# Kernel tuning notes

Hardware: AMD Instinct MI355X
Metric: run time of the kernel (lower is better)

The kernel has to match this reference:

```python
import jax, jax.numpy as jnp
import numpy as np

N_NODES = 50000
N_EDGES = 400000
IN, HID, OUT = 256, 64, 64
HEADS = (8, 8, 1)
NEG_SLOPE = 0.2


def setup_inputs() -> dict:
    key = jax.random.key(0)
    ks = jax.random.split(key, 16)
    def lin(k, fi, fo):
        return jax.random.normal(k, (fi, fo), jnp.float32) / np.sqrt(fi)
    H0, H1, H2 = HEADS
    return {
        "x": jax.random.normal(ks[0], (N_NODES, IN), jnp.float32),
        "src": jax.random.randint(ks[1], (N_EDGES,), 0, N_NODES),
        "dst": jax.random.randint(ks[2], (N_EDGES,), 0, N_NODES),
        # layer 0: in=256 -> (8 heads, 64)
        "W1": lin(ks[3], IN, H0 * HID),
        "al1": 0.1 * jax.random.normal(ks[4], (H0, HID), jnp.float32),
        "ar1": 0.1 * jax.random.normal(ks[5], (H0, HID), jnp.float32),
        "b1": jnp.zeros((H0 * HID,), jnp.float32),
        # layer 1: in=512 -> (8 heads, 64), identity residual (512 == 8*64)
        "W2": lin(ks[6], H0 * HID, H1 * HID),
        "al2": 0.1 * jax.random.normal(ks[7], (H1, HID), jnp.float32),
        "ar2": 0.1 * jax.random.normal(ks[8], (H1, HID), jnp.float32),
        "b2": jnp.zeros((H1 * HID,), jnp.float32),
        # layer 2: in=512 -> (1 head, 64), linear residual projection
        "W3": lin(ks[9], H1 * HID, H2 * OUT),
        "al3": 0.1 * jax.random.normal(ks[10], (H2, OUT), jnp.float32),
        "ar3": 0.1 * jax.random.normal(ks[11], (H2, OUT), jnp.float32),
        "b3": jnp.zeros((H2 * OUT,), jnp.float32),
        "Wr3": lin(ks[12], H1 * HID, H2 * OUT),
    }


def _gat_conv(h, src, dst, W, al, ar, b, res, act):
    # DGL GATConv on a homogeneous graph (feat_src == feat_dst).
    N = h.shape[0]
    H, D = al.shape
    f = (h @ W).reshape(N, H, D)                       # [N,H,D]
    el = jnp.sum(f * al[None], axis=-1)                # [N,H]
    er = jnp.sum(f * ar[None], axis=-1)                # [N,H]
    e = jax.nn.leaky_relu(el[src] + er[dst], NEG_SLOPE)  # [E,H]
    # segment softmax over incoming edges of each dst node
    m = jax.ops.segment_max(e, dst, num_segments=N)    # [N,H]
    ex = jnp.exp(e - m[dst])
    denom = jax.ops.segment_sum(ex, dst, num_segments=N)
    alpha = ex / denom[dst]                            # [E,H]
    msg = f[src] * alpha[:, :, None]                   # [E,H,D]
    rst = jax.ops.segment_sum(msg, dst, num_segments=N)  # [N,H,D]
    if res is not None:
        rst = rst + res
    rst = rst + b.reshape(1, H, D)
    return act(rst) if act is not None else rst


def reference(x, src, dst, W1, al1, ar1, b1, W2, al2, ar2, b2,
              W3, al3, ar3, b3, Wr3):
    N = x.shape[0]
    h = _gat_conv(x, src, dst, W1, al1, ar1, b1, None, jax.nn.elu)
    h = h.reshape(N, -1)                               # flatten(1)
    res2 = h.reshape(N, HEADS[1], HID)                 # identity residual
    h = _gat_conv(h, src, dst, W2, al2, ar2, b2, res2, jax.nn.elu)
    h = h.reshape(N, -1)
    res3 = (h @ Wr3).reshape(N, HEADS[2], OUT)         # projected residual
    h = _gat_conv(h, src, dst, W3, al3, ar3, b3, res3, None)
    return h.mean(axis=1)                              # mean over heads
```

## Files before the change

### kernel.cpp

```cpp
#include <hip/hip_runtime.h>
#include <hip/hip_bf16.h>

#define N_NODES 50000
#define M_PAD 50048
#define N_EDGES 400000
#define SCAN_B 256

typedef __attribute__((ext_vector_type(8))) short short8;
typedef __attribute__((ext_vector_type(4))) float f32x4;

__device__ __forceinline__ unsigned short f2b(float f) {
    unsigned u = __float_as_uint(f);
    return (unsigned short)((u + 0x7fffu + ((u >> 16) & 1u)) >> 16);
}
__device__ __forceinline__ float blo(unsigned u) { return __uint_as_float(u << 16); }
__device__ __forceinline__ float bhi(unsigned u) { return __uint_as_float(u & 0xffff0000u); }

__device__ __forceinline__ void gload_lds16(const void* g, void* l) {
    __builtin_amdgcn_global_load_lds(
        (const __attribute__((address_space(1))) unsigned int*)g,
        (__attribute__((address_space(3))) unsigned int*)l, 16, 0, 0);
}

#define X4_N (N_NODES * 64)
#define W1_SZ (512 * 256)
#define W2_SZ (512 * 512)
#define W3_SZ (64 * 512)
#define WTOT (W1_SZ + W2_SZ + 2 * W3_SZ)
__global__ __launch_bounds__(256) void prep_k(const float* __restrict__ x,
                                              const float* __restrict__ W1,
                                              const float* __restrict__ W2,
                                              const float* __restrict__ W3,
                                              const float* __restrict__ Wr3,
                                              const int* __restrict__ dst,
                                              unsigned short* __restrict__ xb,
                                              unsigned short* __restrict__ Wt1,
                                              unsigned short* __restrict__ Wt2,
                                              unsigned short* __restrict__ Wt3,
                                              int* __restrict__ deg) {
    int i = blockIdx.x * blockDim.x + threadIdx.x;
    if (i < X4_N) {
        float4 v = *(const float4*)&x[(size_t)i * 4];
        unsigned short o[4] = {f2b(v.x), f2b(v.y), f2b(v.z), f2b(v.w)};
        *(ushort2*)&xb[(size_t)i * 4] = make_ushort2(o[0], o[1]);
        *(ushort2*)&xb[(size_t)i * 4 + 2] = make_ushort2(o[2], o[3]);
        return;
    }
    int o = i - X4_N;
    if (o < W1_SZ) {
        int n = o / 256, k = o % 256;
        Wt1[o] = f2b(W1[(size_t)k * 512 + n]);
    } else if (o < W1_SZ + W2_SZ) {
        int oo = o - W1_SZ;
        int n = oo / 512, k = oo % 512;
        Wt2[oo] = f2b(W2[(size_t)k * 512 + n]);
    } else if (o < W1_SZ + W2_SZ + W3_SZ) {
        int oo = o - W1_SZ - W2_SZ;
        int n = oo / 512, k = oo % 512;
        Wt3[oo] = f2b(W3[(size_t)k * 64 + n]);
    } else if (o < WTOT) {
        int oo = o - W1_SZ - W2_SZ - W3_SZ;
        int n = oo / 512, k = oo % 512;
        Wt3[W3_SZ + oo] = f2b(Wr3[(size_t)k * 64 + n]);
    } else {
        int e = o - WTOT;
        if (e < N_EDGES) atomicAdd(&deg[dst[e]], 1);
    }
}

template <int H, int NBX, bool ELER>
__global__ __launch_bounds__(256, 2) void gemm_mfma(const unsigned short* __restrict__ A,
                                                    const unsigned short* __restrict__ Bt,
                                                    unsigned short* __restrict__ C,
                                                    const float* __restrict__ al,
                                                    const float* __restrict__ ar,
                                                    float* __restrict__ el,
                                                    float* __restrict__ er,
                                                    int M, int NN, int K) {
    const int nby = (M + 127) >> 7;
    int bid = blockIdx.x;
    int r, c;
    if (NBX == 4) {
        int full = nby & ~7;
        int nfull = full * 4;
        if (bid < nfull) {
            r = (bid >> 5) * 8 + (bid & 7);
            c = (bid >> 3) & 3;
        } else {
            int t = bid - nfull, rem = nby - full;
            r = full + t % rem;
            c = t / rem;
        }
    } else {
        r = bid;
        c = 0;
    }
    __shared__ unsigned short As[128 * 32];
    __shared__ unsigned short Bs[128 * 32];
    const int tid = threadIdx.x;
    const int w = tid >> 6, l = tid & 63;
    const int bm = r * 128, bn = c * 128;
    const int wr = w >> 1, wc = w & 1;
    const int rA = l >> 2;
    const int kA = (l & 3) * 8;
    const int fr = l & 15, fq = l >> 4;
    f32x4 acc[4][4] = {};

    for (int k0 = 0; k0 < K; k0 += 32) {
#pragma unroll
        for (int j = 0; j < 2; ++j) {
            int row = w * 32 + j * 16 + rA;
            gload_lds16(&A[(size_t)(bm + row) * K + k0 + kA], &As[(w * 2 + j) * 512]);
            gload_lds16(&Bt[(size_t)(bn + row) * K + k0 + kA], &Bs[(w * 2 + j) * 512]);
        }
        __syncthreads();
        short8 a[4], b[4];
#pragma unroll
        for (int m = 0; m < 4; ++m)
            a[m] = *(const short8*)&As[(wr * 64 + m * 16 + fr) * 32 + fq * 8];
#pragma unroll
        for (int n = 0; n < 4; ++n)
            b[n] = *(const short8*)&Bs[(wc * 64 + n * 16 + fr) * 32 + fq * 8];
#pragma unroll
        for (int m = 0; m < 4; ++m)
#pragma unroll
            for (int n = 0; n < 4; ++n)
                acc[m][n] = __builtin_amdgcn_mfma_f32_16x16x32_bf16(a[m], b[n], acc[m][n], 0, 0, 0);
        __syncthreads();
    }

    if (ELER) {
        const int head = (bn >> 6) + wc;
        if (head < H) {
            float alv[4], arv[4];
#pragma unroll
            for (int n = 0; n < 4; ++n) {
                alv[n] = al[head * 64 + n * 16 + fr];
                arv[n] = ar[head * 64 + n * 16 + fr];
            }
#pragma unroll
            for (int m = 0; m < 4; ++m) {
#pragma unroll
                for (int j = 0; j < 4; ++j) {
                    float pl = acc[m][0][j] * alv[0] + acc[m][1][j] * alv[1] +
                               acc[m][2][j] * alv[2] + acc[m][3][j] * alv[3];
                    float pr = acc[m][0][j] * arv[0] + acc[m][1][j] * arv[1] +
                               acc[m][2][j] * arv[2] + acc[m][3][j] * arv[3];
#pragma unroll
                    for (int off = 1; off < 16; off <<= 1) {
                        pl += __shfl_xor(pl, off);
                        pr += __shfl_xor(pr, off);
                    }
                    int rr = bm + wr * 64 + m * 16 + fq * 4 + j;
                    if (fr == 0 && rr < M) {
                        el[(size_t)rr * H + head] = pl;
                        er[(size_t)rr * H + head] = pr;
                    }
                }
            }
        }
    }

#pragma unroll
    for (int m = 0; m < 4; ++m) {
#pragma unroll
        for (int j = 0; j < 4; ++j) {
            int rr = bm + wr * 64 + m * 16 + fq * 4 + j;
            if (rr < M) {
#pragma unroll
                for (int n = 0; n < 4; ++n)
                    C[(size_t)rr * NN + bn + wc * 64 + n * 16 + fr] = f2b(acc[m][n][j]);
            }
        }
    }
}

__global__ __launch_bounds__(SCAN_B) void scan_blocks(const int* __restrict__ in,
                                                      int* __restrict__ out,
                                                      int* __restrict__ part, int n) {
    __shared__ int tmp[SCAN_B];
    int t = threadIdx.x, g = blockIdx.x * SCAN_B + t;
    int v = (g < n) ? in[g] : 0;
    tmp[t] = v;
    __syncthreads();
    for (int off = 1; off < SCAN_B; off <<= 1) {
        int add = (t >= off) ? tmp[t - off] : 0;
        __syncthreads();
        tmp[t] += add;
        __syncthreads();
    }
    if (g < n) out[g] = tmp[t] - v;
    if (t == SCAN_B - 1) part[blockIdx.x] = tmp[t];
}

__global__ __launch_bounds__(SCAN_B) void scan_part(int* __restrict__ part, int n) {
    __shared__ int tmp[SCAN_B];
    int t = threadIdx.x;
    int v = (t < n) ? part[t] : 0;
    tmp[t] = v;
    __syncthreads();
    for (int off = 1; off < SCAN_B; off <<= 1) {
        int add = (t >= off) ? tmp[t - off] : 0;
        __syncthreads();
        tmp[t] += add;
        __syncthreads();
    }
    if (t < n) part[t] = tmp[t] - v;
}

__global__ __launch_bounds__(256) void add_off(int* __restrict__ rowptr,
                                               int* __restrict__ cursor,
                                               const int* __restrict__ part,
                                               int* __restrict__ csr_src,
                                               int n, int E) {
    int g = blockIdx.x * blockDim.x + threadIdx.x;
    if (g < n) {
        int v = rowptr[g] + part[g / SCAN_B];
        rowptr[g] = v;
        cursor[g] = v;
    }
    if (g == 0) rowptr[n] = E;
    if (g < 8) csr_src[E + g] = 0;
}

__global__ __launch_bounds__(256) void scatter_k(const int* __restrict__ src,
                                                 const int* __restrict__ dst,
                                                 int* __restrict__ cursor,
                                                 int* __restrict__ csr_src, int E) {
    int e = blockIdx.x * blockDim.x + threadIdx.x;
    if (e < E) {
        int p = atomicAdd(&cursor[dst[e]], 1);
        csr_src[p] = src[e];
    }
}

template <bool HAS_INIT>
__global__ __launch_bounds__(256) void gat_agg8(const unsigned short* __restrict__ f,
                                                const float* __restrict__ el,
                                                const float* __restrict__ er,
                                                const int* __restrict__ rowptr,
                                                const int* __restrict__ csr_src,
                                                const unsigned short* __restrict__ init,
                                                const float* __restrict__ bias,
                                                unsigned short* __restrict__ outb, int N) {
    int w = (blockIdx.x * blockDim.x + threadIdx.x) >> 6;
    int lane = threadIdx.x & 63;
    if (w >= N) return;
    const int d = w;
    const int s0 = rowptr[d], s1 = rowptr[d + 1];
    const int hh = lane & 7;
    const int esub = lane >> 3;
    const int myhead = lane >> 3;
    const int sl8 = lane * 8;
    const float erh = er[(size_t)d * 8 + hh];

    int snj[8];
#pragma unroll
    for (int j = 0; j < 8; ++j)
        snj[j] = csr_src[(s0 + j < s1) ? (s0 + j) : N_EDGES];
    uint4 pk[8];
#pragma unroll
    for (int j = 0; j < 8; ++j)
        pk[j] = *(const uint4*)&f[(size_t)snj[j] * 512 + sl8];

    bool valid0 = s0 + esub < s1;
    float v0 = el[(size_t)snj[esub] * 8 + hh] + erh;
    v0 = v0 > 0.f ? v0 : 0.2f * v0;
    float mx = valid0 ? v0 : -1e30f;
    for (int i = s0 + 8 + esub; i < s1; i += 8) {
        float v = el[(size_t)csr_src[i] * 8 + hh] + erh;
        v = v > 0.f ? v : 0.2f * v;
        mx = fmaxf(mx, v);
    }
    mx = fmaxf(mx, __shfl_xor(mx, 8));
    mx = fmaxf(mx, __shfl_xor(mx, 16));
    mx = fmaxf(mx, __shfl_xor(mx, 32));

    float am0 = valid0 ? __expf(v0 - mx) : 0.f;
    float sm = am0;
    float acc[8] = {};
#pragma unroll
    for (int j = 0; j < 8; ++j) {
        float alpha = __shfl(am0, (j << 3) | myhead);
        acc[0] += blo(pk[j].x) * alpha;
        acc[1] += bhi(pk[j].x) * alpha;
        acc[2] += blo(pk[j].y) * alpha;
        acc[3] += bhi(pk[j].y) * alpha;
        acc[4] += blo(pk[j].z) * alpha;
        acc[5] += bhi(pk[j].z) * alpha;
        acc[6] += blo(pk[j].w) * alpha;
        acc[7] += bhi(pk[j].w) * alpha;
    }

    for (int ii = s0 + 8; ii < s1; ii += 8) {
        int sn2[8];
#pragma unroll
        for (int j = 0; j < 8; ++j)
            sn2[j] = csr_src[(ii + j < s1) ? (ii + j) : N_EDGES];
        uint4 qk[8];
#pragma unroll
        for (int j = 0; j < 8; ++j)
            qk[j] = *(const uint4*)&f[(size_t)sn2[j] * 512 + sl8];
        bool valid = ii + esub < s1;
        float v = el[(size_t)sn2[esub] * 8 + hh] + erh;
        v = v > 0.f ? v : 0.2f * v;
        float am = valid ? __expf(v - mx) : 0.f;
        sm += am;
#pragma unroll
        for (int j = 0; j < 8; ++j) {
            float alpha = __shfl(am, (j << 3) | myhead);
            acc[0] += blo(qk[j].x) * alpha;
            acc[1] += bhi(qk[j].x) * alpha;
            acc[2] += blo(qk[j].y) * alpha;
            acc[3] += bhi(qk[j].y) * alpha;
            acc[4] += blo(qk[j].z) * alpha;
            acc[5] += bhi(qk[j].z) * alpha;
            acc[6] += blo(qk[j].w) * alpha;
            acc[7] += bhi(qk[j].w) * alpha;
        }
    }

    sm += __shfl_xor(sm, 8);
    sm += __shfl_xor(sm, 16);
    sm += __shfl_xor(sm, 32);
    float smh = __shfl(sm, myhead);
    float inv = smh > 0.f ? 1.0f / smh : 0.f;
#pragma unroll
    for (int j = 0; j < 8; ++j) acc[j] *= inv;

    const int sl = (lane & 7) * 8;
    float4 b0 = *(const float4*)&bias[myhead * 64 + sl];
    float4 b1 = *(const float4*)&bias[myhead * 64 + sl + 4];
    float bb[8] = {b0.x, b0.y, b0.z, b0.w, b1.x, b1.y, b1.z, b1.w};
    if (HAS_INIT) {
        uint4 iv = *(const uint4*)&init[(size_t)d * 512 + sl8];
        acc[0] += blo(iv.x); acc[1] += bhi(iv.x);
        acc[2] += blo(iv.y); acc[3] += bhi(iv.y);
        acc[4] += blo(iv.z); acc[5] += bhi(iv.z);
        acc[6] += blo(iv.w); acc[7] += bhi(iv.w);
    }
    unsigned short ob[8];
#pragma unroll
    for (int j = 0; j < 8; ++j) {
        float v = acc[j] + bb[j];
        v = v > 0.f ? v : __expf(v) - 1.f;
        ob[j] = f2b(v);
    }
    uint4 ov;
    ov.x = (unsigned)ob[0] | ((unsigned)ob[1] << 16);
    ov.y = (unsigned)ob[2] | ((unsigned)ob[3] << 16);
    ov.z = (unsigned)ob[4] | ((unsigned)ob[5] << 16);
    ov.w = (unsigned)ob[6] | ((unsigned)ob[7] << 16);
    *(uint4*)&outb[(size_t)d * 512 + sl8] = ov;
}

__global__ __launch_bounds__(256) void gat_agg1(const unsigned short* __restrict__ f,
                                                const float* __restrict__ el,
                                                const float* __restrict__ er,
                                                const int* __restrict__ rowptr,
                                                const int* __restrict__ csr_src,
                                                const float* __restrict__ bias,
                                                float* __restrict__ outf, int N) {
    int w = (blockIdx.x * blockDim.x + threadIdx.x) >> 6;
    int lane = threadIdx.x & 63;
    if (w >= N) return;
    const int d = w;
    const int s0 = rowptr[d], s1 = rowptr[d + 1];
    const int esub = lane >> 3, sl = (lane & 7) * 8;
    const float erh = er[d];

    int snj[8];
#pragma unroll
    for (int j = 0; j < 8; ++j)
        snj[j] = csr_src[(s0 + j < s1) ? (s0 + j) : N_EDGES];
    int sn0 = snj[esub];
    uint4 pk0 = *(const uint4*)&f[(size_t)sn0 * 128 + sl];

    bool valid0 = s0 + esub < s1;
    float v0 = el[sn0] + erh;
    v0 = v0 > 0.f ? v0 : 0.2f * v0;
    float mx = valid0 ? v0 : -1e30f;
    for (int i = s0 + 8 + esub; i < s1; i += 8) {
        float v = el[csr_src[i]] + erh;
        v = v > 0.f ? v : 0.2f * v;
        mx = fmaxf(mx, v);
    }
    mx = fmaxf(mx, __shfl_xor(mx, 8));
    mx = fmaxf(mx, __shfl_xor(mx, 16));
    mx = fmaxf(mx, __shfl_xor(mx, 32));

    float am0 = valid0 ? __expf(v0 - mx) : 0.f;
    float sm = am0;
    float acc[8];
    acc[0] = blo(pk0.x) * am0; acc[1] = bhi(pk0.x) * am0;
    acc[2] = blo(pk0.y) * am0; acc[3] = bhi(pk0.y) * am0;
    acc[4] = blo(pk0.z) * am0; acc[5] = bhi(pk0.z) * am0;
    acc[6] = blo(pk0.w) * am0; acc[7] = bhi(pk0.w) * am0;

    for (int ii = s0 + 8; ii < s1; ii += 8) {
        int i = ii + esub;
        bool valid = i < s1;
        int sn = csr_src[valid ? i : N_EDGES];
        uint4 pk = *(const uint4*)&f[(size_t)sn * 128 + sl];
        float v = el[sn] + erh;
        v = v > 0.f ? v : 0.2f * v;
        float am = valid ? __expf(v - mx) : 0.f;
        sm += am;
        acc[0] += blo(pk.x) * am; acc[1] += bhi(pk.x) * am;
        acc[2] += blo(pk.y) * am; acc[3] += bhi(pk.y) * am;
        acc[4] += blo(pk.z) * am; acc[5] += bhi(pk.z) * am;
        acc[6] += blo(pk.w) * am; acc[7] += bhi(pk.w) * am;
    }

    sm += __shfl_xor(sm, 8);
    sm += __shfl_xor(sm, 16);
    sm += __shfl_xor(sm, 32);
#pragma unroll
    for (int off = 8; off < 64; off <<= 1)
#pragma unroll
        for (int j = 0; j < 8; ++j) acc[j] += __shfl_xor(acc[j], off);
    float inv = sm > 0.f ? 1.0f / sm : 0.f;

    if (esub == 0) {
        uint4 rv = *(const uint4*)&f[(size_t)d * 128 + 64 + sl];
        float rr[8] = {blo(rv.x), bhi(rv.x), blo(rv.y), bhi(rv.y),
                       blo(rv.z), bhi(rv.z), blo(rv.w), bhi(rv.w)};
#pragma unroll
        for (int j = 0; j < 8; ++j)
            outf[(size_t)d * 64 + sl + j] = acc[j] * inv + bias[sl + j] + rr[j];
    }
}

extern "C" void kernel_launch(void* const* d_in, const int* in_sizes, int n_in,
                              void* d_out, int out_size, void* d_ws, size_t ws_size,
                              hipStream_t stream) {
    const float* x   = (const float*)d_in[0];
    const int*   src = (const int*)d_in[1];
    const int*   dst = (const int*)d_in[2];
    const float* W1  = (const float*)d_in[3];
    const float* al1 = (const float*)d_in[4];
    const float* ar1 = (const float*)d_in[5];
    const float* b1  = (const float*)d_in[6];
    const float* W2  = (const float*)d_in[7];
    const float* al2 = (const float*)d_in[8];
    const float* ar2 = (const float*)d_in[9];
    const float* b2  = (const float*)d_in[10];
    const float* W3  = (const float*)d_in[11];
    const float* al3 = (const float*)d_in[12];
    const float* ar3 = (const float*)d_in[13];
    const float* b3  = (const float*)d_in[14];
    const float* Wr3 = (const float*)d_in[15];
    float* out = (float*)d_out;

    unsigned short* xb   = (unsigned short*)d_ws;
    unsigned short* fb   = xb + (size_t)M_PAD * 256;
    unsigned short* h1b  = fb + (size_t)M_PAD * 512;
    unsigned short* h2b  = h1b + (size_t)M_PAD * 512;
    unsigned short* f3r  = h2b + (size_t)M_PAD * 512;
    unsigned short* Wt1  = f3r + (size_t)M_PAD * 128;
    unsigned short* Wt2  = Wt1 + 512 * 256;
    unsigned short* Wt3  = Wt2 + 512 * 512;
    float* el = (float*)(Wt3 + 128 * 512);
    float* er = el + (size_t)N_NODES * 8;
    int* rowptr  = (int*)(er + (size_t)N_NODES * 8);
    int* cursor  = rowptr + (N_NODES + 1);
    int* part    = cursor + N_NODES;
    int* csr_src = part + 256;

    const dim3 blk(256);
    const int E = N_EDGES, N = N_NODES;
    const int nb = (N + SCAN_B - 1) / SCAN_B;
    const int gy = (N + 127) / 128;

    hipMemsetAsync(cursor, 0, (size_t)N * 4, stream);
    prep_k<<<(X4_N + WTOT + E + 255) / 256, blk, 0, stream>>>(
        x, W1, W2, W3, Wr3, dst, xb, Wt1, Wt2, Wt3, cursor);
    scan_blocks<<<nb, SCAN_B, 0, stream>>>(cursor, rowptr, part, N);
    scan_part<<<1, SCAN_B, 0, stream>>>(part, nb);
    add_off<<<nb, blk, 0, stream>>>(rowptr, cursor, part, csr_src, N, E);
    scatter_k<<<(E + 255) / 256, blk, 0, stream>>>(src, dst, cursor, csr_src, E);

    gemm_mfma<8, 4, true><<<4 * gy, blk, 0, stream>>>(
        xb, Wt1, fb, al1, ar1, el, er, N, 512, 256);
    gat_agg8<false><<<(N + 3) / 4, blk, 0, stream>>>(
        fb, el, er, rowptr, csr_src, nullptr, b1, h1b, N);

    gemm_mfma<8, 4, true><<<4 * gy, blk, 0, stream>>>(
        h1b, Wt2, fb, al2, ar2, el, er, N, 512, 512);
    gat_agg8<true><<<(N + 3) / 4, blk, 0, stream>>>(
        fb, el, er, rowptr, csr_src, h1b, b2, h2b, N);

    gemm_mfma<1, 1, true><<<gy, blk, 0, stream>>>(
        h2b, Wt3, f3r, al3, ar3, el, er, N, 128, 512);
    gat_agg1<<<(N + 3) / 4, blk, 0, stream>>>(
        f3r, el, er, rowptr, csr_src, b3, out, N);
}
```

Before: 343.7 us.

## Use 128x256 tile GEMM with 512 threads for the 8-head layers

Result: no change. 350.5 us (+2.0%).

```diff
diff --git a/kernel.cpp b/kernel.cpp
--- a/kernel.cpp
+++ b/kernel.cpp
@@ -68,7 +68,99 @@
     }
 }
 
-template <int H, int NBX, bool ELER>
+template <int H>
+__global__ __launch_bounds__(512) void gemm256(const unsigned short* __restrict__ A,
+                                               const unsigned short* __restrict__ Bt,
+                                               unsigned short* __restrict__ C,
+                                               const float* __restrict__ al,
+                                               const float* __restrict__ ar,
+                                               float* __restrict__ el,
+                                               float* __restrict__ er,
+                                               int M, int NN, int K) {
+    const int nby = (M + 127) >> 7;
+    const int tiles = nby * 2;
+    const int chunk = (tiles + 7) >> 3;
+    const int x = blockIdx.x & 7, q = blockIdx.x >> 3;
+    const int t = x * chunk + q;
+    if (t >= tiles) return;
+    const int r = t >> 1, c = t & 1;
+    __shared__ unsigned short As[128 * 32];
+    __shared__ unsigned short Bs[256 * 32];
+    const int tid = threadIdx.x;
+    const int w = tid >> 6, l = tid & 63;
+    const int bm = r * 128, bn = c * 256;
+    const int wr = w >> 2, wc = w & 3;
+    const int fr = l & 15, fq = l >> 4;
+    const int lr = l >> 2, lk = (l & 3) * 8;
+    f32x4 acc[4][4] = {};
+
+    for (int k0 = 0; k0 < K; k0 += 32) {
+        gload_lds16(&A[(size_t)(bm + w * 16 + lr) * K + k0 + lk], &As[w * 512]);
+        gload_lds16(&Bt[(size_t)(bn + w * 16 + lr) * K + k0 + lk], &Bs[w * 512]);
+        gload_lds16(&Bt[(size_t)(bn + 128 + w * 16 + lr) * K + k0 + lk], &Bs[4096 + w * 512]);
+        __syncthreads();
+        short8 a[4], b[4];
+#pragma unroll
+        for (int m = 0; m < 4; ++m)
+            a[m] = *(const short8*)&As[(wr * 64 + m * 16 + fr) * 32 + fq * 8];
+#pragma unroll
+        for (int n = 0; n < 4; ++n)
+            b[n] = *(const short8*)&Bs[(wc * 64 + n * 16 + fr) * 32 + fq * 8];
+#pragma unroll
+        for (int m = 0; m < 4; ++m)
+#pragma unroll
+            for (int n = 0; n < 4; ++n)
+                acc[m][n] = __builtin_amdgcn_mfma_f32_16x16x32_bf16(a[m], b[n], acc[m][n], 0, 0, 0);
+        __syncthreads();
+    }
+
+    {
+        const int head = (bn >> 6) + wc;
+        if (head < H) {
+            float alv[4], arv[4];
+#pragma unroll
+            for (int n = 0; n < 4; ++n) {
+                alv[n] = al[head * 64 + n * 16 + fr];
+                arv[n] = ar[head * 64 + n * 16 + fr];
+            }
+#pragma unroll
+            for (int m = 0; m < 4; ++m) {
+#pragma unroll
+                for (int j = 0; j < 4; ++j) {
+                    float pl = acc[m][0][j] * alv[0] + acc[m][1][j] * alv[1] +
+                               acc[m][2][j] * alv[2] + acc[m][3][j] * alv[3];
+                    float pr = acc[m][0][j] * arv[0] + acc[m][1][j] * arv[1] +
+                               acc[m][2][j] * arv[2] + acc[m][3][j] * arv[3];
+#pragma unroll
+                    for (int off = 1; off < 16; off <<= 1) {
+                        pl += __shfl_xor(pl, off);
+                        pr += __shfl_xor(pr, off);
+                    }
+                    int rr = bm + wr * 64 + m * 16 + fq * 4 + j;
+                    if (fr == 0 && rr < M) {
+                        el[(size_t)rr * H + head] = pl;
+                        er[(size_t)rr * H + head] = pr;
+                    }
+                }
+            }
+        }
+    }
+
+#pragma unroll
+    for (int m = 0; m < 4; ++m) {
+#pragma unroll
+        for (int j = 0; j < 4; ++j) {
+            int rr = bm + wr * 64 + m * 16 + fq * 4 + j;
+            if (rr < M) {
+#pragma unroll
+                for (int n = 0; n < 4; ++n)
+                    C[(size_t)rr * NN + bn + wc * 64 + n * 16 + fr] = f2b(acc[m][n][j]);
+            }
+        }
+    }
+}
+
+template <int H>
 __global__ __launch_bounds__(256, 2) void gemm_mfma(const unsigned short* __restrict__ A,
                                                     const unsigned short* __restrict__ Bt,
                                                     unsigned short* __restrict__ C,
@@ -77,24 +169,7 @@
                                                     float* __restrict__ el,
                                                     float* __restrict__ er,
                                                     int M, int NN, int K) {
-    const int nby = (M + 127) >> 7;
-    int bid = blockIdx.x;
-    int r, c;
-    if (NBX == 4) {
-        int full = nby & ~7;
-        int nfull = full * 4;
-        if (bid < nfull) {
-            r = (bid >> 5) * 8 + (bid & 7);
-            c = (bid >> 3) & 3;
-        } else {
-            int t = bid - nfull, rem = nby - full;
-            r = full + t % rem;
-            c = t / rem;
-        }
-    } else {
-        r = bid;
-        c = 0;
-    }
+    int r = blockIdx.x, c = 0;
     __shared__ unsigned short As[128 * 32];
     __shared__ unsigned short Bs[128 * 32];
     const int tid = threadIdx.x;
@@ -129,7 +204,7 @@
         __syncthreads();
     }
 
-    if (ELER) {
+    {
         const int head = (bn >> 6) + wc;
         if (head < H) {
             float alv[4], arv[4];
@@ -471,6 +546,8 @@
     const int E = N_EDGES, N = N_NODES;
     const int nb = (N + SCAN_B - 1) / SCAN_B;
     const int gy = (N + 127) / 128;
+    const int tiles = gy * 2;
+    const int g256 = 8 * ((tiles + 7) / 8);
 
     hipMemsetAsync(cursor, 0, (size_t)N * 4, stream);
     prep_k<<<(X4_N + WTOT + E + 255) / 256, blk, 0, stream>>>(
@@ -480,17 +557,17 @@
     add_off<<<nb, blk, 0, stream>>>(rowptr, cursor, part, csr_src, N, E);
     scatter_k<<<(E + 255) / 256, blk, 0, stream>>>(src, dst, cursor, csr_src, E);
 
-    gemm_mfma<8, 4, true><<<4 * gy, blk, 0, stream>>>(
+    gemm256<8><<<g256, dim3(512), 0, stream>>>(
         xb, Wt1, fb, al1, ar1, el, er, N, 512, 256);
     gat_agg8<false><<<(N + 3) / 4, blk, 0, stream>>>(
         fb, el, er, rowptr, csr_src, nullptr, b1, h1b, N);
 
-    gemm_mfma<8, 4, true><<<4 * gy, blk, 0, stream>>>(
+    gemm256<8><<<g256, dim3(512), 0, stream>>>(
         h1b, Wt2, fb, al2, ar2, el, er, N, 512, 512);
     gat_agg8<true><<<(N + 3) / 4, blk, 0, stream>>>(
         fb, el, er, rowptr, csr_src, h1b, b2, h2b, N);
 
-    gemm_mfma<1, 1, true><<<gy, blk, 0, stream>>>(
+    gemm_mfma<1><<<gy, blk, 0, stream>>>(
         h2b, Wt3, f3r, al3, ar3, el, er, N, 128, 512);
     gat_agg1<<<(N + 3) / 4, blk, 0, stream>>>(
         f3r, el, er, rowptr, csr_src, b3, out, N);
```
